# Performance work log

Hardware: AMD Instinct MI355X
Metric: run time of the kernel (lower is better)

Reference implementation:

```python
import jax, jax.numpy as jnp
import numpy as np

B, S, N = 8, 4096, 512
K_DIM, HEADS, WS = 512, 8, 128
HD = K_DIM // HEADS


def setup_inputs() -> dict:
    key = jax.random.key(0)
    ks = jax.random.split(key, 9)
    sc = 0.02
    return {
        "inputs": jax.random.normal(ks[0], (B, S, N), dtype=jnp.float32),
        "Wq": jax.random.normal(ks[1], (K_DIM, N), dtype=jnp.float32) * sc,
        "bq": jax.random.normal(ks[2], (K_DIM,), dtype=jnp.float32) * sc,
        "Wk": jax.random.normal(ks[3], (K_DIM, N), dtype=jnp.float32) * sc,
        "bk": jax.random.normal(ks[4], (K_DIM,), dtype=jnp.float32) * sc,
        "Wv": jax.random.normal(ks[5], (K_DIM, N), dtype=jnp.float32) * sc,
        "bv": jax.random.normal(ks[6], (K_DIM,), dtype=jnp.float32) * sc,
        "Wp": jax.random.normal(ks[7], (N, K_DIM), dtype=jnp.float32) * sc,
        "bp": jax.random.normal(ks[8], (N,), dtype=jnp.float32) * sc,
    }


def reference(inputs, Wq, bq, Wk, bk, Wv, bv, Wp, bp):
    b, s, n = inputs.shape
    nw = s // WS  # number of windows per sequence
    # QKV projections (torch Linear: x @ W.T + b)
    q = inputs @ Wq.T + bq  # [B,S,K]
    k = inputs @ Wk.T + bk
    v = inputs @ Wv.T + bv

    def to_windows(t):
        # [B,S,K] -> [B*nw, H, WS, HD]
        t = t.reshape(b * nw, WS, HEADS, HD)
        return t.transpose(0, 2, 1, 3)

    q, k, v = to_windows(q), to_windows(k), to_windows(v)
    scale = HD ** (-0.5)
    # windowed attention: [BW,H,WS,WS]
    score = jnp.einsum('whqd,whkd->whqk', q, k) * scale
    attn = jax.nn.softmax(score, axis=-1)  # dropout is identity in eval
    out = jnp.einsum('whqk,whkd->whqd', attn, v)  # [BW,H,WS,HD]
    out = out.transpose(0, 2, 1, 3).reshape(b, s, K_DIM)  # window reverse
    out = out @ Wp.T + bp  # [B,S,N]
    return out
```

## Files before the change

kernel.cpp:

```cpp
#include <hip/hip_runtime.h>
#include <hip/hip_bf16.h>
#include <stdint.h>


typedef __bf16 bf16;
typedef __bf16 bf16x8 __attribute__((ext_vector_type(8)));
typedef __bf16 bf16x4 __attribute__((ext_vector_type(4)));
typedef float  f32x4  __attribute__((ext_vector_type(4)));

#define DEV static __device__ __forceinline__

DEV void gld_lds16(const bf16* g, bf16* l) {
  __builtin_amdgcn_global_load_lds(
      (__attribute__((address_space(1))) void*)(g),
      (__attribute__((address_space(3))) void*)(l), 16, 0, 0);
}

__global__ void cast_x(const float* __restrict__ x, bf16* __restrict__ xb, int n4) {
  int i = blockIdx.x * blockDim.x + threadIdx.x;
  if (i < n4) {
    float4 v = ((const float4*)x)[i];
    bf16x4 o;
    o[0] = (bf16)v.x; o[1] = (bf16)v.y; o[2] = (bf16)v.z; o[3] = (bf16)v.w;
    ((bf16x4*)xb)[i] = o;
  }
}

__global__ void cast_w(const float* __restrict__ Wq, const float* __restrict__ Wk,
                       const float* __restrict__ Wv, const float* __restrict__ Wp,
                       bf16* __restrict__ dst) {
  int i = (blockIdx.x * blockDim.x + threadIdx.x) * 4;
  const float* src;
  int off;
  if (i < 786432) {
    int seg = i >> 18;
    off = i & 262143;
    src = (seg == 0) ? Wq : ((seg == 1) ? Wk : Wv);
  } else {
    off = i - 786432;
    src = Wp;
  }
  float4 v = *(const float4*)(src + off);
  bf16x4 o;
  o[0] = (bf16)v.x; o[1] = (bf16)v.y; o[2] = (bf16)v.z; o[3] = (bf16)v.w;
  *(bf16x4*)(dst + i) = o;
}

template <bool BF16OUT>
__global__ __launch_bounds__(256, 2)
void gemm_bt(const bf16* __restrict__ A, const bf16* __restrict__ B,
             const float* __restrict__ bias0, const float* __restrict__ bias1,
             const float* __restrict__ bias2, void* __restrict__ Cout, int Ntot) {
  __shared__ bf16 As[128 * 32];
  __shared__ bf16 Bs[128 * 32];
  const int tid = threadIdx.x;
  const int wave = tid >> 6, lane = tid & 63;
  const int wm = wave >> 1, wn = wave & 1;
  const int lane15 = lane & 15, quad = lane >> 4;
  const long row0 = (long)blockIdx.x * 128;
  const long col0 = (long)blockIdx.y * 128;

  f32x4 acc[4][4] = {};

  const int sr = lane >> 2;
  const int sc = (lane & 3) * 8;

  for (int k0 = 0; k0 < 512; k0 += 32) {
    __syncthreads();
    for (int i = 0; i < 2; ++i) {
      int ch = wave * 2 + i;
      gld_lds16(A + (row0 + ch * 16 + sr) * 512 + k0 + sc, As + ch * 512 + lane * 8);
      gld_lds16(B + (col0 + ch * 16 + sr) * 512 + k0 + sc, Bs + ch * 512 + lane * 8);
    }
    __syncthreads();
    bf16x8 af[4], bfr[4];
    for (int r = 0; r < 4; ++r)
      af[r] = *(const bf16x8*)(As + (wm * 64 + r * 16 + lane15) * 32 + quad * 8);
    for (int c = 0; c < 4; ++c)
      bfr[c] = *(const bf16x8*)(Bs + (wn * 64 + c * 16 + lane15) * 32 + quad * 8);
    for (int r = 0; r < 4; ++r)
      for (int c = 0; c < 4; ++c)
        acc[r][c] = __builtin_amdgcn_mfma_f32_16x16x32_bf16(af[r], bfr[c], acc[r][c], 0, 0, 0);
  }

  for (int r = 0; r < 4; ++r) {
    int lrow = wm * 64 + r * 16 + quad * 4;
    for (int c = 0; c < 4; ++c) {
      long col = col0 + wn * 64 + c * 16 + lane15;
      int seg = (int)(col >> 9);
      const float* bsel = (seg == 0) ? bias0 : ((seg == 1) ? bias1 : bias2);
      float bias = bsel[col & 511];
      for (int g = 0; g < 4; ++g) {
        long row = row0 + lrow + g;
        float v = acc[r][c][g] + bias;
        if (BF16OUT) ((bf16*)Cout)[row * Ntot + col] = (bf16)v;
        else        ((float*)Cout)[row * Ntot + col] = v;
      }
    }
  }
}

__global__ __launch_bounds__(256, 2)
void attn_win(const bf16* __restrict__ QKV, bf16* __restrict__ Out) {
  __shared__ __align__(16) char smem[34816 + 16384];
  bf16* Qs = (bf16*)smem;
  bf16* Ks = Qs + 128 * 64;
  bf16* Ps = (bf16*)smem;
  bf16* Vt = (bf16*)(smem + 34816);

  const int tid = threadIdx.x;
  const int wave = tid >> 6, lane = tid & 63;
  const int lane15 = lane & 15, quad = lane >> 4;
  const int win = blockIdx.x >> 3, head = blockIdx.x & 7;

  const bf16* Qg = QKV + (size_t)win * 128 * 1536 + head * 64;
  const bf16* Kg = Qg + 512;
  const bf16* Vg = Qg + 1024;

  {
    const int r8 = lane >> 3;
    const int c8 = (lane & 7) * 8;
    for (int i = 0; i < 4; ++i) {
      int ch = wave * 4 + i;
      gld_lds16(Qg + (size_t)(ch * 8 + r8) * 1536 + c8, Qs + ch * 512 + lane * 8);
      gld_lds16(Kg + (size_t)(ch * 8 + r8) * 1536 + c8, Ks + ch * 512 + lane * 8);
    }
  }
  for (int i = 0; i < 4; ++i) {
    int q = i * 256 + tid;
    int t = q & 127, d0 = (q >> 7) * 8;
    bf16x8 v = *(const bf16x8*)(Vg + (size_t)t * 1536 + d0);
    for (int j = 0; j < 8; ++j) Vt[(d0 + j) * 128 + t] = v[j];
  }
  __syncthreads();

  f32x4 accs[2][8] = {};
  for (int c = 0; c < 8; ++c) {
    bf16x8 b0 = *(const bf16x8*)(Ks + (c * 16 + lane15) * 64 + quad * 8);
    bf16x8 b1 = *(const bf16x8*)(Ks + (c * 16 + lane15) * 64 + 32 + quad * 8);
    for (int r = 0; r < 2; ++r) {
      bf16x8 a0 = *(const bf16x8*)(Qs + (wave * 32 + r * 16 + lane15) * 64 + quad * 8);
      bf16x8 a1 = *(const bf16x8*)(Qs + (wave * 32 + r * 16 + lane15) * 64 + 32 + quad * 8);
      accs[r][c] = __builtin_amdgcn_mfma_f32_16x16x32_bf16(a0, b0, accs[r][c], 0, 0, 0);
      accs[r][c] = __builtin_amdgcn_mfma_f32_16x16x32_bf16(a1, b1, accs[r][c], 0, 0, 0);
    }
  }
  __syncthreads();

  const float scale = 0.125f;
  for (int r = 0; r < 2; ++r) {
    for (int g = 0; g < 4; ++g) {
      float m = -1e30f;
      for (int c = 0; c < 8; ++c) m = fmaxf(m, accs[r][c][g]);
      for (int mk = 1; mk <= 8; mk <<= 1) m = fmaxf(m, __shfl_xor(m, mk, 64));
      float sum = 0.f;
      for (int c = 0; c < 8; ++c) {
        float e = __expf((accs[r][c][g] - m) * scale);
        accs[r][c][g] = e;
        sum += e;
      }
      for (int mk = 1; mk <= 8; mk <<= 1) sum += __shfl_xor(sum, mk, 64);
      float inv = 1.0f / sum;
      int prow = wave * 32 + r * 16 + quad * 4 + g;
      for (int c = 0; c < 8; ++c)
        Ps[prow * 136 + c * 16 + lane15] = (bf16)(accs[r][c][g] * inv);
    }
  }
  __syncthreads();

  f32x4 acco[2][4] = {};
  for (int kk = 0; kk < 4; ++kk) {
    bf16x8 a[2];
    for (int r = 0; r < 2; ++r)
      a[r] = *(const bf16x8*)(Ps + (wave * 32 + r * 16 + lane15) * 136 + kk * 32 + quad * 8);
    for (int c = 0; c < 4; ++c) {
      bf16x8 b = *(const bf16x8*)(Vt + (c * 16 + lane15) * 128 + kk * 32 + quad * 8);
      for (int r = 0; r < 2; ++r)
        acco[r][c] = __builtin_amdgcn_mfma_f32_16x16x32_bf16(a[r], b, acco[r][c], 0, 0, 0);
    }
  }

  bf16* Og = Out + (size_t)win * 128 * 512 + head * 64;
  for (int r = 0; r < 2; ++r) {
    int row = wave * 32 + r * 16 + quad * 4;
    for (int c = 0; c < 4; ++c) {
      int col = c * 16 + lane15;
      for (int g = 0; g < 4; ++g)
        Og[(size_t)(row + g) * 512 + col] = (bf16)acco[r][c][g];
    }
  }
}

extern "C" void kernel_launch(void* const* d_in, const int* in_sizes, int n_in,
                              void* d_out, int out_size, void* d_ws, size_t ws_size,
                              hipStream_t stream) {
  const float* x  = (const float*)d_in[0];
  const float* Wq = (const float*)d_in[1];
  const float* bq = (const float*)d_in[2];
  const float* Wk = (const float*)d_in[3];
  const float* bk = (const float*)d_in[4];
  const float* Wv = (const float*)d_in[5];
  const float* bv = (const float*)d_in[6];
  const float* Wp = (const float*)d_in[7];
  const float* bp = (const float*)d_in[8];

  bf16* Xb    = (bf16*)d_ws;
  bf16* Wqkvb = Xb + 16777216;
  bf16* Wpb   = Wqkvb + 786432;
  bf16* QKVb  = Wpb + 262144;
  bf16* AttnB = QKVb + 50331648;

  cast_x<<<16384, 256, 0, stream>>>(x, Xb, 4194304);
  cast_w<<<1024, 256, 0, stream>>>(Wq, Wk, Wv, Wp, Wqkvb);
  gemm_bt<true><<<dim3(256, 12), 256, 0, stream>>>(Xb, Wqkvb, bq, bk, bv, QKVb, 1536);
  attn_win<<<2048, 256, 0, stream>>>(QKVb, AttnB);
  gemm_bt<false><<<dim3(256, 4), 256, 0, stream>>>(AttnB, Wpb, bp, bp, bp, d_out, 512);
}
```

Baseline: 268.2 us.

## Swizzle LDS layouts, widen GEMM K-tile to 64, pair V transpose stores

The GEMM now stages 64-wide K tiles with an XOR swizzle on the 16-byte column groups, which halves the number of barrier pairs and is meant to avoid LDS bank conflicts on the MFMA fragment reads. The attention kernel applies the same swizzle to its Q/K tiles and hoists the Q fragments out of the loop. It also transposes V using paired 4-byte stores into a swizzled layout instead of scalar 2-byte stores. The cost is more index arithmetic and double the GEMM LDS footprint, which could limit occupancy.

```diff
diff --git a/kernel.cpp b/kernel.cpp
--- a/kernel.cpp
+++ b/kernel.cpp
@@ -6,6 +6,7 @@
 typedef __bf16 bf16;
 typedef __bf16 bf16x8 __attribute__((ext_vector_type(8)));
 typedef __bf16 bf16x4 __attribute__((ext_vector_type(4)));
+typedef __bf16 bf16x2 __attribute__((ext_vector_type(2)));
 typedef float  f32x4  __attribute__((ext_vector_type(4)));
 
 #define DEV static __device__ __forceinline__
@@ -51,8 +52,8 @@
 void gemm_bt(const bf16* __restrict__ A, const bf16* __restrict__ B,
              const float* __restrict__ bias0, const float* __restrict__ bias1,
              const float* __restrict__ bias2, void* __restrict__ Cout, int Ntot) {
-  __shared__ bf16 As[128 * 32];
-  __shared__ bf16 Bs[128 * 32];
+  __shared__ bf16 As[128 * 64];
+  __shared__ bf16 Bs[128 * 64];
   const int tid = threadIdx.x;
   const int wave = tid >> 6, lane = tid & 63;
   const int wm = wave >> 1, wn = wave & 1;
@@ -62,25 +63,31 @@
 
   f32x4 acc[4][4] = {};
 
-  const int sr = lane >> 2;
-  const int sc = (lane & 3) * 8;
-
-  for (int k0 = 0; k0 < 512; k0 += 32) {
+  const int srow = lane >> 3;
+  const int sg = (lane & 7) ^ srow;
+
+  for (int k0 = 0; k0 < 512; k0 += 64) {
     __syncthreads();
-    for (int i = 0; i < 2; ++i) {
-      int ch = wave * 2 + i;
-      gld_lds16(A + (row0 + ch * 16 + sr) * 512 + k0 + sc, As + ch * 512 + lane * 8);
-      gld_lds16(B + (col0 + ch * 16 + sr) * 512 + k0 + sc, Bs + ch * 512 + lane * 8);
+    for (int i = 0; i < 4; ++i) {
+      int r0 = (wave * 4 + i) * 8;
+      gld_lds16(A + (row0 + r0 + srow) * 512 + k0 + sg * 8, As + r0 * 64 + lane * 8);
+      gld_lds16(B + (col0 + r0 + srow) * 512 + k0 + sg * 8, Bs + r0 * 64 + lane * 8);
     }
     __syncthreads();
-    bf16x8 af[4], bfr[4];
-    for (int r = 0; r < 4; ++r)
-      af[r] = *(const bf16x8*)(As + (wm * 64 + r * 16 + lane15) * 32 + quad * 8);
-    for (int c = 0; c < 4; ++c)
-      bfr[c] = *(const bf16x8*)(Bs + (wn * 64 + c * 16 + lane15) * 32 + quad * 8);
-    for (int r = 0; r < 4; ++r)
-      for (int c = 0; c < 4; ++c)
-        acc[r][c] = __builtin_amdgcn_mfma_f32_16x16x32_bf16(af[r], bfr[c], acc[r][c], 0, 0, 0);
+    for (int s = 0; s < 2; ++s) {
+      bf16x8 af[4], bfr[4];
+      for (int r = 0; r < 4; ++r) {
+        int row = wm * 64 + r * 16 + lane15;
+        af[r] = *(const bf16x8*)(As + row * 64 + (((s * 4 + quad) ^ (lane15 & 7)) * 8));
+      }
+      for (int c = 0; c < 4; ++c) {
+        int row = wn * 64 + c * 16 + lane15;
+        bfr[c] = *(const bf16x8*)(Bs + row * 64 + (((s * 4 + quad) ^ (lane15 & 7)) * 8));
+      }
+      for (int r = 0; r < 4; ++r)
+        for (int c = 0; c < 4; ++c)
+          acc[r][c] = __builtin_amdgcn_mfma_f32_16x16x32_bf16(af[r], bfr[c], acc[r][c], 0, 0, 0);
+    }
   }
 
   for (int r = 0; r < 4; ++r) {
@@ -118,31 +125,46 @@
   const bf16* Vg = Qg + 1024;
 
   {
-    const int r8 = lane >> 3;
-    const int c8 = (lane & 7) * 8;
+    const int srow = lane >> 3;
+    const int sg = (lane & 7) ^ srow;
     for (int i = 0; i < 4; ++i) {
-      int ch = wave * 4 + i;
-      gld_lds16(Qg + (size_t)(ch * 8 + r8) * 1536 + c8, Qs + ch * 512 + lane * 8);
-      gld_lds16(Kg + (size_t)(ch * 8 + r8) * 1536 + c8, Ks + ch * 512 + lane * 8);
-    }
-  }
-  for (int i = 0; i < 4; ++i) {
-    int q = i * 256 + tid;
-    int t = q & 127, d0 = (q >> 7) * 8;
-    bf16x8 v = *(const bf16x8*)(Vg + (size_t)t * 1536 + d0);
-    for (int j = 0; j < 8; ++j) Vt[(d0 + j) * 128 + t] = v[j];
+      int r0 = (wave * 4 + i) * 8;
+      gld_lds16(Qg + (size_t)(r0 + srow) * 1536 + sg * 8, Qs + r0 * 64 + lane * 8);
+      gld_lds16(Kg + (size_t)(r0 + srow) * 1536 + sg * 8, Ks + r0 * 64 + lane * 8);
+    }
+  }
+  for (int it = 0; it < 2; ++it) {
+    int q = it * 256 + tid;
+    int tp = q >> 3;
+    int d0 = (q & 7) * 8;
+    bf16x8 v0 = *(const bf16x8*)(Vg + (size_t)(2 * tp) * 1536 + d0);
+    bf16x8 v1 = *(const bf16x8*)(Vg + (size_t)(2 * tp + 1) * 1536 + d0);
+    int gt = tp >> 2, po = tp & 3;
+    for (int j = 0; j < 8; ++j) {
+      int d = d0 + j;
+      int p = gt ^ ((d >> 3) ^ (d & 7));
+      bf16x2 pr;
+      pr[0] = v0[j]; pr[1] = v1[j];
+      *(bf16x2*)(Vt + d * 128 + p * 8 + po * 2) = pr;
+    }
   }
   __syncthreads();
 
   f32x4 accs[2][8] = {};
-  for (int c = 0; c < 8; ++c) {
-    bf16x8 b0 = *(const bf16x8*)(Ks + (c * 16 + lane15) * 64 + quad * 8);
-    bf16x8 b1 = *(const bf16x8*)(Ks + (c * 16 + lane15) * 64 + 32 + quad * 8);
-    for (int r = 0; r < 2; ++r) {
-      bf16x8 a0 = *(const bf16x8*)(Qs + (wave * 32 + r * 16 + lane15) * 64 + quad * 8);
-      bf16x8 a1 = *(const bf16x8*)(Qs + (wave * 32 + r * 16 + lane15) * 64 + 32 + quad * 8);
-      accs[r][c] = __builtin_amdgcn_mfma_f32_16x16x32_bf16(a0, b0, accs[r][c], 0, 0, 0);
-      accs[r][c] = __builtin_amdgcn_mfma_f32_16x16x32_bf16(a1, b1, accs[r][c], 0, 0, 0);
+  {
+    bf16x8 aq[2][2];
+    for (int r = 0; r < 2; ++r)
+      for (int s = 0; s < 2; ++s) {
+        int row = wave * 32 + r * 16 + lane15;
+        aq[r][s] = *(const bf16x8*)(Qs + row * 64 + (((s * 4 + quad) ^ (lane15 & 7)) * 8));
+      }
+    for (int c = 0; c < 8; ++c) {
+      int row = c * 16 + lane15;
+      for (int s = 0; s < 2; ++s) {
+        bf16x8 bk = *(const bf16x8*)(Ks + row * 64 + (((s * 4 + quad) ^ (lane15 & 7)) * 8));
+        accs[0][c] = __builtin_amdgcn_mfma_f32_16x16x32_bf16(aq[0][s], bk, accs[0][c], 0, 0, 0);
+        accs[1][c] = __builtin_amdgcn_mfma_f32_16x16x32_bf16(aq[1][s], bk, accs[1][c], 0, 0, 0);
+      }
     }
   }
   __syncthreads();
@@ -174,7 +196,9 @@
     for (int r = 0; r < 2; ++r)
       a[r] = *(const bf16x8*)(Ps + (wave * 32 + r * 16 + lane15) * 136 + kk * 32 + quad * 8);
     for (int c = 0; c < 4; ++c) {
-      bf16x8 b = *(const bf16x8*)(Vt + (c * 16 + lane15) * 128 + kk * 32 + quad * 8);
+      int d = c * 16 + lane15;
+      int p = (kk * 4 + quad) ^ ((d >> 3) ^ (d & 7));
+      bf16x8 b = *(const bf16x8*)(Vt + d * 128 + p * 8);
       for (int r = 0; r < 2; ++r)
         acco[r][c] = __builtin_amdgcn_mfma_f32_16x16x32_bf16(a[r], b, acco[r][c], 0, 0, 0);
     }
```

New measurement: 252.1 us. -6.0%, faster.
